# Kernel optimization log

Measured on AMD Instinct MI355X. Metric: run time of the kernel, lower is better.

Reference implementation:

```python
import jax, jax.numpy as jnp
import numpy as np

N_NODES = 50000
N_EDGES = 600000
D_IN = 44


def _glorot(key, shape):
    fan_in = shape[0]
    return jax.random.normal(key, shape, jnp.float32) * (1.0 / np.sqrt(fan_in))


def setup_inputs() -> dict:
    key = jax.random.key(0)
    ks = jax.random.split(key, 12)
    x = jax.random.normal(ks[0], (N_NODES, D_IN), jnp.float32)
    edge_index = jax.random.randint(ks[1], (2, N_EDGES), 0, N_NODES, dtype=jnp.int64)
    return {
        "x": x,
        "edge_index": edge_index,
        "W1": _glorot(ks[2], (D_IN, 128)),  "b1": jnp.zeros((128,), jnp.float32),
        "W2": _glorot(ks[3], (128, 64)),    "b2": jnp.zeros((64,), jnp.float32),
        "W3": _glorot(ks[4], (64, 32)),     "b3": jnp.zeros((32,), jnp.float32),
        "Wf1": _glorot(ks[5], (32, 16)),    "bf1": jnp.zeros((16,), jnp.float32),
        "Wf2": _glorot(ks[6], (16, 1)),     "bf2": jnp.zeros((1,), jnp.float32),
    }


def _gcn_conv(x, W, b, src, dst, norm, n):
    # GCNConv: h = x @ W; out_i = sum_{j->i} norm_ij * h_j  (self-loops included in src/dst)
    h = x @ W
    msg = h[src] * norm[:, None]              # [E+N, d_out] gather + scale
    out = jax.ops.segment_sum(msg, dst, num_segments=n)  # scatter-add
    return out + b


def reference(x, edge_index, W1, b1, W2, b2, W3, b3, Wf1, bf1, Wf2, bf2):
    n = x.shape[0]
    loop = jnp.arange(n, dtype=edge_index.dtype)
    src = jnp.concatenate([edge_index[0], loop])
    dst = jnp.concatenate([edge_index[1], loop])
    # symmetric normalization deg^-1/2 A_hat deg^-1/2 (deg includes self-loops)
    deg = jax.ops.segment_sum(jnp.ones_like(dst, dtype=x.dtype), dst, num_segments=n)
    dinv = jax.lax.rsqrt(jnp.maximum(deg, 1.0))
    norm = dinv[src] * dinv[dst]

    h = jax.nn.relu(_gcn_conv(x, W1, b1, src, dst, norm, n))
    h = jax.nn.relu(_gcn_conv(h, W2, b2, src, dst, norm, n))
    h = jax.nn.relu(_gcn_conv(h, W3, b3, src, dst, norm, n))
    h = jax.nn.relu(h @ Wf1 + bf1)
    return jax.nn.sigmoid(h @ Wf2 + bf2)
```

## Files before the change

### kernel.cpp

```cpp
#include <hip/hip_runtime.h>
#include <hip/hip_bf16.h>
#include <hip/hip_fp16.h>
#include <math.h>

#define N_NODES 50000
#define N_EDGES 600000
#define D_IN    44


__device__ __forceinline__ unsigned pack_bf2(float a, float b) {
    unsigned ua = __float_as_uint(a);
    ua = (ua + 0x7fffu + ((ua >> 16) & 1u)) >> 16;
    unsigned ub = __float_as_uint(b);
    ub = (ub + 0x7fffu + ((ub >> 16) & 1u)) & 0xffff0000u;
    return ua | ub;
}

#define BL(u) __uint_as_float((u) << 16)
#define BH(u) __uint_as_float((u) & 0xffff0000u)


__global__ void k_packx(const float* __restrict__ x, unsigned* __restrict__ xh,
                        int npairs, int* __restrict__ degc, int n) {
    int i = blockIdx.x * blockDim.x + threadIdx.x;
    if (i < npairs) {
        float2 v = ((const float2*)x)[i];
        xh[i] = pack_bf2(v.x, v.y);
    }
    if (i < n) degc[i] = 0;
}

__global__ void k_count(const int* __restrict__ dst, int* degc, int e) {
    int i = blockIdx.x * blockDim.x + threadIdx.x;
    if (i < e) atomicAdd(&degc[dst[i]], 1);
}

__global__ void k_blocksum(const int* __restrict__ degc, int* __restrict__ bsum, int n) {
    int i = blockIdx.x * 256 + threadIdx.x;
    int v = (i < n) ? degc[i] : 0;
    #pragma unroll
    for (int off = 32; off > 0; off >>= 1) v += __shfl_down(v, off, 64);
    __shared__ int ws[4];
    if ((threadIdx.x & 63) == 0) ws[threadIdx.x >> 6] = v;
    __syncthreads();
    if (threadIdx.x == 0) bsum[blockIdx.x] = ws[0] + ws[1] + ws[2] + ws[3];
}

__global__ void k_rowptr(const int* __restrict__ degc, const int* __restrict__ bsum,
                         int* __restrict__ row_ptr, int* __restrict__ cursor,
                         float* __restrict__ dinv, int n, int nb) {
    __shared__ int sb[256];
    __shared__ int s[256];
    int t = threadIdx.x;

    int bv = (t < nb) ? bsum[t] : 0;
    sb[t] = bv;
    __syncthreads();
    #pragma unroll
    for (int off = 1; off < 256; off <<= 1) {
        int u = (t >= off) ? sb[t - off] : 0;
        __syncthreads();
        sb[t] += u;
        __syncthreads();
    }
    int prefix = (blockIdx.x == 0) ? 0 : sb[blockIdx.x - 1];

    int i = blockIdx.x * 256 + t;
    int d = (i < n) ? degc[i] : 0;
    s[t] = d;
    __syncthreads();
    #pragma unroll
    for (int off = 1; off < 256; off <<= 1) {
        int u = (t >= off) ? s[t - off] : 0;
        __syncthreads();
        s[t] += u;
        __syncthreads();
    }
    int ex = s[t] - d + prefix;
    if (i < n) {
        row_ptr[i] = ex;
        cursor[i]  = ex;
        dinv[i]    = rsqrtf(1.0f + (float)d);
        if (i == n - 1) row_ptr[n] = ex + d;
    }
}

__global__ void k_fill(const int* __restrict__ src, const int* __restrict__ dst,
                       const float* __restrict__ dinv, int* cursor,
                       unsigned* __restrict__ csr_ew, int e) {
    int i = blockIdx.x * blockDim.x + threadIdx.x;
    if (i < e) {
        int s = src[i], d = dst[i];
        int p = atomicAdd(&cursor[d], 1);
        __half h = __float2half(dinv[s] * dinv[d]);
        csr_ew[p] = (unsigned)s | ((unsigned)__half_as_ushort(h) << 16);
    }
}


#define AGG_EDGE_HDR(EW, lo, hi)                                                \
            unsigned e0 = EW[min(k + 0, (hi) - 1)];                             \
            unsigned e1 = EW[min(k + 1, (hi) - 1)];                             \
            unsigned e2 = EW[min(k + 2, (hi) - 1)];                             \
            unsigned e3 = EW[min(k + 3, (hi) - 1)];                             \
            unsigned e4 = EW[min(k + 4, (hi) - 1)];                             \
            unsigned e5 = EW[min(k + 5, (hi) - 1)];                             \
            unsigned e6 = EW[min(k + 6, (hi) - 1)];                             \
            unsigned e7 = EW[min(k + 7, (hi) - 1)];                             \
            float w0 = __half2float(__ushort_as_half((unsigned short)(e0 >> 16)));                     \
            float w1 = (k + 1 < (hi)) ? __half2float(__ushort_as_half((unsigned short)(e1 >> 16))) : 0.0f;\
            float w2 = (k + 2 < (hi)) ? __half2float(__ushort_as_half((unsigned short)(e2 >> 16))) : 0.0f;\
            float w3 = (k + 3 < (hi)) ? __half2float(__ushort_as_half((unsigned short)(e3 >> 16))) : 0.0f;\
            float w4 = (k + 4 < (hi)) ? __half2float(__ushort_as_half((unsigned short)(e4 >> 16))) : 0.0f;\
            float w5 = (k + 5 < (hi)) ? __half2float(__ushort_as_half((unsigned short)(e5 >> 16))) : 0.0f;\
            float w6 = (k + 6 < (hi)) ? __half2float(__ushort_as_half((unsigned short)(e6 >> 16))) : 0.0f;\
            float w7 = (k + 7 < (hi)) ? __half2float(__ushort_as_half((unsigned short)(e7 >> 16))) : 0.0f;


#define AGG_ACC(tv, wv)                                   \
        acc.x += wv * BL(tv.x);                           \
        acc.y += wv * BH(tv.x);                           \
        acc.z += wv * BL(tv.y);                           \
        acc.w += wv * BH(tv.y);

#define AGG_BODY(T2, W4, lo, hi, j, acc, EW)                                    \
    {                                                                           \
        for (int k = (lo); k < (hi); k += 8) {                                  \
            AGG_EDGE_HDR(EW, lo, hi)                                            \
            uint2 t0 = T2[(size_t)(e0 & 0xffffu) * (W4) + (j)];                 \
            uint2 t1 = T2[(size_t)(e1 & 0xffffu) * (W4) + (j)];                 \
            uint2 t2 = T2[(size_t)(e2 & 0xffffu) * (W4) + (j)];                 \
            uint2 t3 = T2[(size_t)(e3 & 0xffffu) * (W4) + (j)];                 \
            uint2 t4 = T2[(size_t)(e4 & 0xffffu) * (W4) + (j)];                 \
            uint2 t5 = T2[(size_t)(e5 & 0xffffu) * (W4) + (j)];                 \
            uint2 t6 = T2[(size_t)(e6 & 0xffffu) * (W4) + (j)];                 \
            uint2 t7 = T2[(size_t)(e7 & 0xffffu) * (W4) + (j)];                 \
            AGG_ACC(t0, w0) AGG_ACC(t1, w1) AGG_ACC(t2, w2) AGG_ACC(t3, w3)     \
            AGG_ACC(t4, w4) AGG_ACC(t5, w5) AGG_ACC(t6, w6) AGG_ACC(t7, w7)     \
        }                                                                       \
    }


#define AGG_ACC4(tv, wv)                                  \
        a0.x += wv * BL(tv.x); a0.y += wv * BH(tv.x);     \
        a0.z += wv * BL(tv.y); a0.w += wv * BH(tv.y);     \
        a1.x += wv * BL(tv.z); a1.y += wv * BH(tv.z);     \
        a1.z += wv * BL(tv.w); a1.w += wv * BH(tv.w);

#define AGG_BODY4(T4, W4, lo, hi, j, EW)                                        \
    {                                                                           \
        for (int k = (lo); k < (hi); k += 8) {                                  \
            AGG_EDGE_HDR(EW, lo, hi)                                            \
            uint4 t0 = T4[(size_t)(e0 & 0xffffu) * (W4) + (j)];                 \
            uint4 t1 = T4[(size_t)(e1 & 0xffffu) * (W4) + (j)];                 \
            uint4 t2 = T4[(size_t)(e2 & 0xffffu) * (W4) + (j)];                 \
            uint4 t3 = T4[(size_t)(e3 & 0xffffu) * (W4) + (j)];                 \
            uint4 t4 = T4[(size_t)(e4 & 0xffffu) * (W4) + (j)];                 \
            uint4 t5 = T4[(size_t)(e5 & 0xffffu) * (W4) + (j)];                 \
            uint4 t6 = T4[(size_t)(e6 & 0xffffu) * (W4) + (j)];                 \
            uint4 t7 = T4[(size_t)(e7 & 0xffffu) * (W4) + (j)];                 \
            AGG_ACC4(t0, w0) AGG_ACC4(t1, w1) AGG_ACC4(t2, w2) AGG_ACC4(t3, w3) \
            AGG_ACC4(t4, w4) AGG_ACC4(t5, w5) AGG_ACC4(t6, w6) AGG_ACC4(t7, w7) \
        }                                                                       \
    }


#define AGG1_ECAP 1536

__global__ void k_agg1(const unsigned* __restrict__ T, const float* __restrict__ dinv,
                       const int* __restrict__ row_ptr, const unsigned* __restrict__ csr_ew,
                       unsigned short* __restrict__ O, int n) {
    __shared__ unsigned csr_s[AGG1_ECAP];
    const int t = threadIdx.x;
    const int base = blockIdx.x * 256;
    const int g0 = base / 11;
    const int glast = min((base + 255) / 11, n - 1);
    const int lo_blk = row_ptr[g0];
    const int nume = row_ptr[glast + 1] - lo_blk;
    const unsigned* ep;
    if (nume <= AGG1_ECAP) {
        for (int i = t; i < nume; i += 256) csr_s[i] = csr_ew[lo_blk + i];
        ep = csr_s;
    } else {
        ep = csr_ew + lo_blk;
    }
    __syncthreads();

    int idx = base + t;
    if (idx >= n * 11) return;
    int g = idx / 11;
    int j = idx - g * 11;

    const uint2* T2 = (const uint2*)T;
    float di = dinv[g];
    float sw = di * di;
    uint2 sv = T2[(size_t)g * 11 + j];
    float4 acc;
    acc.x = sw * BL(sv.x);
    acc.y = sw * BH(sv.x);
    acc.z = sw * BL(sv.y);
    acc.w = sw * BH(sv.y);
    int lo = row_ptr[g] - lo_blk;
    int hi = row_ptr[g + 1] - lo_blk;
    AGG_BODY(T2, 11, lo, hi, j, acc, ep)
    uint2 o;
    o.x = pack_bf2(acc.x, acc.y);
    o.y = pack_bf2(acc.z, acc.w);
    ((uint2*)O)[(size_t)g * 11 + j] = o;
}


template<int DI, int DO, int CT, bool BIAS_RELU, bool IN_BF16, bool OUT_BF16>
__global__ void k_gemm(const void* __restrict__ Xv, const float* __restrict__ W,
                       const float* __restrict__ b, void* __restrict__ H, int n) {
    const int ct0 = blockIdx.y * CT;
    int node = blockIdx.x * blockDim.x + threadIdx.x;
    if (node >= n) return;

    float acc[CT];
    #pragma unroll
    for (int c = 0; c < CT; ++c) acc[c] = BIAS_RELU ? b[ct0 + c] : 0.0f;

    const float* Wb = W + ct0;
    #pragma unroll
    for (int k0 = 0; k0 < DI / 4; ++k0) {
        float x0, x1, x2, x3;
        if (IN_BF16) {
            uint2 xv = ((const uint2*)((const unsigned short*)Xv + (size_t)node * DI))[k0];
            x0 = BL(xv.x); x1 = BH(xv.x); x2 = BL(xv.y); x3 = BH(xv.y);
        } else {
            float4 xv = ((const float4*)((const float*)Xv + (size_t)node * DI))[k0];
            x0 = xv.x; x1 = xv.y; x2 = xv.z; x3 = xv.w;
        }
        #pragma unroll
        for (int c = 0; c < CT; ++c) acc[c] += x0 * Wb[(k0 * 4 + 0) * DO + c];
        #pragma unroll
        for (int c = 0; c < CT; ++c) acc[c] += x1 * Wb[(k0 * 4 + 1) * DO + c];
        #pragma unroll
        for (int c = 0; c < CT; ++c) acc[c] += x2 * Wb[(k0 * 4 + 2) * DO + c];
        #pragma unroll
        for (int c = 0; c < CT; ++c) acc[c] += x3 * Wb[(k0 * 4 + 3) * DO + c];
    }

    #pragma unroll
    for (int c4 = 0; c4 < CT / 4; ++c4) {
        float4 v;
        v.x = acc[c4 * 4 + 0]; v.y = acc[c4 * 4 + 1];
        v.z = acc[c4 * 4 + 2]; v.w = acc[c4 * 4 + 3];
        if (BIAS_RELU) {
            v.x = fmaxf(v.x, 0.0f); v.y = fmaxf(v.y, 0.0f);
            v.z = fmaxf(v.z, 0.0f); v.w = fmaxf(v.w, 0.0f);
        }
        if (OUT_BF16) {
            uint2 p;
            p.x = pack_bf2(v.x, v.y);
            p.y = pack_bf2(v.z, v.w);
            ((uint2*)((unsigned short*)H + (size_t)node * DO + ct0))[c4] = p;
        } else {
            ((float4*)((float*)H + (size_t)node * DO + ct0))[c4] = v;
        }
    }
}


#define F23_ECAP 2048

__global__ void __launch_bounds__(256) k_fused23(
        const unsigned* __restrict__ T, const float* __restrict__ dinv,
        const int* __restrict__ row_ptr, const unsigned* __restrict__ csr_ew,
        const float* __restrict__ b2, const float* __restrict__ W3,
        unsigned short* __restrict__ outH, int n) {
    __shared__ unsigned csr_s[F23_ECAP];
    __shared__ float Xs[32 * 68];
    const int t = threadIdx.x;
    const int m = t >> 3;
    const int j = t & 7;
    const int g = blockIdx.x * 32 + m;
    const int gm = min(g, n - 1);

    const int g0 = blockIdx.x * 32;
    const int glast = min(g0 + 31, n - 1);
    const int lo_blk = row_ptr[g0];
    const int nume = row_ptr[glast + 1] - lo_blk;
    const unsigned* ep;
    if (nume <= F23_ECAP) {
        for (int i = t; i < nume; i += 256) csr_s[i] = csr_ew[lo_blk + i];
        ep = csr_s;
    } else {
        ep = csr_ew + lo_blk;
    }
    __syncthreads();

    const uint4* T4 = (const uint4*)T;
    {
        float di = dinv[gm];
        float sw = di * di;
        uint4 sv = T4[(size_t)gm * 8 + j];
        float4 a0, a1;
        a0.x = sw * BL(sv.x); a0.y = sw * BH(sv.x);
        a0.z = sw * BL(sv.y); a0.w = sw * BH(sv.y);
        a1.x = sw * BL(sv.z); a1.y = sw * BH(sv.z);
        a1.z = sw * BL(sv.w); a1.w = sw * BH(sv.w);
        int lo = row_ptr[gm] - lo_blk;
        int hi = row_ptr[gm + 1] - lo_blk;
        AGG_BODY4(T4, 8, lo, hi, j, ep)
        float4 bv0 = ((const float4*)b2)[2 * j];
        float4 bv1 = ((const float4*)b2)[2 * j + 1];
        a0.x = fmaxf(a0.x + bv0.x, 0.0f); a0.y = fmaxf(a0.y + bv0.y, 0.0f);
        a0.z = fmaxf(a0.z + bv0.z, 0.0f); a0.w = fmaxf(a0.w + bv0.w, 0.0f);
        a1.x = fmaxf(a1.x + bv1.x, 0.0f); a1.y = fmaxf(a1.y + bv1.y, 0.0f);
        a1.z = fmaxf(a1.z + bv1.z, 0.0f); a1.w = fmaxf(a1.w + bv1.w, 0.0f);
        *(float4*)&Xs[m * 68 + 8 * j]     = a0;
        *(float4*)&Xs[m * 68 + 8 * j + 4] = a1;
    }
    __syncthreads();

    {
        const int c = j * 4;
        float4 o = {0.0f, 0.0f, 0.0f, 0.0f};
        #pragma unroll 4
        for (int k4 = 0; k4 < 16; ++k4) {
            float4 xs = *(const float4*)&Xs[m * 68 + 4 * k4];
#define G3(hs, kk) { float4 wv = *(const float4*)&W3[(kk) * 32 + c];            \
            o.x += (hs) * wv.x; o.y += (hs) * wv.y;                             \
            o.z += (hs) * wv.z; o.w += (hs) * wv.w; }
            G3(xs.x, 4 * k4 + 0) G3(xs.y, 4 * k4 + 1)
            G3(xs.z, 4 * k4 + 2) G3(xs.w, 4 * k4 + 3)
#undef G3
        }
        if (g < n) {
            uint2 ov;
            ov.x = pack_bf2(o.x, o.y);
            ov.y = pack_bf2(o.z, o.w);
            *(uint2*)(outH + (size_t)g * 32 + c) = ov;
        }
    }
}


#define F3M_ECAP 2048

__global__ void __launch_bounds__(128) k_fused3m(
        const unsigned* __restrict__ T, const float* __restrict__ dinv,
        const int* __restrict__ row_ptr, const unsigned* __restrict__ csr_ew,
        const float* __restrict__ b3,
        const float* __restrict__ Wf1, const float* __restrict__ bf1,
        const float* __restrict__ Wf2, const float* __restrict__ bf2,
        float* __restrict__ out, int n) {
    __shared__ unsigned csr_s[F3M_ECAP];
    __shared__ float Xs[32 * 36];
    const int t = threadIdx.x;
    const int m = t >> 2;
    const int j = t & 3;
    const int g = blockIdx.x * 32 + m;
    const int gm = min(g, n - 1);

    const int g0 = blockIdx.x * 32;
    const int glast = min(g0 + 31, n - 1);
    const int lo_blk = row_ptr[g0];
    const int nume = row_ptr[glast + 1] - lo_blk;
    const unsigned* ep;
    if (nume <= F3M_ECAP) {
        for (int i = t; i < nume; i += 128) csr_s[i] = csr_ew[lo_blk + i];
        ep = csr_s;
    } else {
        ep = csr_ew + lo_blk;
    }
    __syncthreads();

    const uint4* T4 = (const uint4*)T;
    {
        float di = dinv[gm];
        float sw = di * di;
        uint4 sv = T4[(size_t)gm * 4 + j];
        float4 a0, a1;
        a0.x = sw * BL(sv.x); a0.y = sw * BH(sv.x);
        a0.z = sw * BL(sv.y); a0.w = sw * BH(sv.y);
        a1.x = sw * BL(sv.z); a1.y = sw * BH(sv.z);
        a1.z = sw * BL(sv.w); a1.w = sw * BH(sv.w);
        int lo = row_ptr[gm] - lo_blk;
        int hi = row_ptr[gm + 1] - lo_blk;
        AGG_BODY4(T4, 4, lo, hi, j, ep)
        float4 bv0 = ((const float4*)b3)[2 * j];
        float4 bv1 = ((const float4*)b3)[2 * j + 1];
        a0.x = fmaxf(a0.x + bv0.x, 0.0f); a0.y = fmaxf(a0.y + bv0.y, 0.0f);
        a0.z = fmaxf(a0.z + bv0.z, 0.0f); a0.w = fmaxf(a0.w + bv0.w, 0.0f);
        a1.x = fmaxf(a1.x + bv1.x, 0.0f); a1.y = fmaxf(a1.y + bv1.y, 0.0f);
        a1.z = fmaxf(a1.z + bv1.z, 0.0f); a1.w = fmaxf(a1.w + bv1.w, 0.0f);
        *(float4*)&Xs[m * 36 + 8 * j]     = a0;
        *(float4*)&Xs[m * 36 + 8 * j + 4] = a1;
    }
    __syncthreads();

    {
        const int c = j * 4;
        float4 h = *(const float4*)&bf1[c];
        #pragma unroll
        for (int k4 = 0; k4 < 8; ++k4) {
            float4 xs = *(const float4*)&Xs[m * 36 + 4 * k4];
#define FM(hs, kk) { float4 wv = *(const float4*)&Wf1[(kk) * 16 + c];           \
            h.x += (hs) * wv.x; h.y += (hs) * wv.y;                             \
            h.z += (hs) * wv.z; h.w += (hs) * wv.w; }
            FM(xs.x, 4 * k4 + 0) FM(xs.y, 4 * k4 + 1)
            FM(xs.z, 4 * k4 + 2) FM(xs.w, 4 * k4 + 3)
#undef FM
        }
        float4 w2 = *(const float4*)&Wf2[c];
        float p = fmaxf(h.x, 0.0f) * w2.x + fmaxf(h.y, 0.0f) * w2.y
                + fmaxf(h.z, 0.0f) * w2.z + fmaxf(h.w, 0.0f) * w2.w;
        p += __shfl_down(p, 2);
        p += __shfl_down(p, 1);
        if (j == 0 && g < n) out[g] = 1.0f / (1.0f + expf(-(p + bf2[0])));
    }
}


extern "C" void kernel_launch(void* const* d_in, const int* in_sizes, int n_in,
                              void* d_out, int out_size, void* d_ws, size_t ws_size,
                              hipStream_t stream) {
    const float* x   = (const float*)d_in[0];
    const int*   ei  = (const int*)d_in[1];
    const float* W1  = (const float*)d_in[2];
    const float* b1  = (const float*)d_in[3];
    const float* W2  = (const float*)d_in[4];
    const float* b2  = (const float*)d_in[5];
    const float* W3  = (const float*)d_in[6];
    const float* b3  = (const float*)d_in[7];
    const float* Wf1 = (const float*)d_in[8];
    const float* bf1 = (const float*)d_in[9];
    const float* Wf2 = (const float*)d_in[10];
    const float* bf2 = (const float*)d_in[11];
    float* out = (float*)d_out;

    const int N = N_NODES, E = N_EDGES;
    const int* src = ei;
    const int* dst = ei + E;

    const int B   = 256;
    const int NB  = (N + B - 1) / B;
    const int NBX = 200;

    char* w = (char*)d_ws;
    float*    dinv    = (float*)w;     w += (size_t)N * 4;
    int*      degc    = (int*)w;       w += (size_t)N * 4;
    int*      row_ptr = (int*)w;       w += (size_t)(N + 4) * 4;
    int*      cursor  = (int*)w;       w += (size_t)N * 4;
    int*      bsum    = (int*)w;       w += (size_t)256 * 4;
    unsigned* csr_ew  = (unsigned*)w;  w += (size_t)E * 4;
    unsigned* xh      = (unsigned*)w;  w += (size_t)N * 44 * 2;
    unsigned short* aggXh = (unsigned short*)w;  w += (size_t)N * 44 * 2;
    float*    buf1    = (float*)w;     w += (size_t)N * 128 * 4;
    unsigned short* bufAh = (unsigned short*)w;  w += (size_t)N * 64 * 2;
    unsigned short* bufBh = (unsigned short*)w;  w += (size_t)N * 32 * 2;

    k_packx    <<<(N * 22 + B - 1) / B, B, 0, stream>>>(x, xh, N * 22, degc, N);
    k_count    <<<(E + B - 1) / B, B, 0, stream>>>(dst, degc, E);
    k_blocksum <<<NB, B, 0, stream>>>(degc, bsum, N);
    k_rowptr   <<<NB, B, 0, stream>>>(degc, bsum, row_ptr, cursor, dinv, N, NB);
    k_fill     <<<(E + B - 1) / B, B, 0, stream>>>(src, dst, dinv, cursor, csr_ew, E);

    k_agg1<<<(N * 11 + B - 1) / B, B, 0, stream>>>(xh, dinv, row_ptr, csr_ew, aggXh, N);
    k_gemm<44, 128, 16, true, true, false><<<dim3(NBX, 8), B, 0, stream>>>(aggXh, W1, b1, buf1, N);
    k_gemm<128, 64, 16, false, false, true><<<dim3(NBX, 4), B, 0, stream>>>(buf1, W2, nullptr, bufAh, N);

    k_fused23<<<(N + 31) / 32, 256, 0, stream>>>((const unsigned*)bufAh, dinv, row_ptr,
                                                 csr_ew, b2, W3, bufBh, N);

    k_fused3m<<<(N + 31) / 32, 128, 0, stream>>>((const unsigned*)bufBh, dinv, row_ptr,
                                                 csr_ew, b3, Wf1, bf1, Wf2, bf2, out, N);
}
```

Measured before the change: 245.3 us.

## Fuse CSR build into cooperative kernel and fuse layer-1/2 GEMMs via LDS

Replaces five separate CSR-construction launches with one cooperative kernel that uses grid-wide syncs between packing, degree counting, the scan and the fill, and computes per-block sums with a second atomic. It also merges the two dense GEMMs into one kernel that keeps the 128-wide ReLU activations in shared memory instead of writing and rereading an fp32 buffer from global memory. This is meant to cut launch overhead and the global traffic of the intermediate. The cost is grid.sync latency, extra atomics on bsum, and shared-memory pressure that may lower occupancy in the fused GEMM.

Result: slower. 875.8 us (+257.0%).

```diff
diff --git a/kernel.cpp b/kernel.cpp
--- a/kernel.cpp
+++ b/kernel.cpp
@@ -1,11 +1,15 @@
 #include <hip/hip_runtime.h>
 #include <hip/hip_bf16.h>
 #include <hip/hip_fp16.h>
+#include <hip/hip_cooperative_groups.h>
 #include <math.h>
+
+namespace cg = cooperative_groups;
 
 #define N_NODES 50000
 #define N_EDGES 600000
 #define D_IN    44
+#define NB_CSR  196
 
 
 __device__ __forceinline__ unsigned pack_bf2(float a, float b) {
@@ -18,6 +22,78 @@
 
 #define BL(u) __uint_as_float((u) << 16)
 #define BH(u) __uint_as_float((u) & 0xffff0000u)
+
+
+__global__ void __launch_bounds__(256) k_csr(
+        const float* __restrict__ x, unsigned* __restrict__ xh,
+        const int* __restrict__ src, const int* __restrict__ dst,
+        int* __restrict__ degc, int* __restrict__ bsum,
+        int* __restrict__ row_ptr, int* __restrict__ cursor,
+        float* __restrict__ dinv, unsigned* __restrict__ csr_ew) {
+    cg::grid_group grid = cg::this_grid();
+    const int nth = gridDim.x * 256;
+    const int tid = blockIdx.x * 256 + threadIdx.x;
+
+    for (int i = tid; i < N_NODES; i += nth) degc[i] = 0;
+    if (tid < 256) bsum[tid] = 0;
+    for (int i = tid; i < N_NODES * 22; i += nth) {
+        float2 v = ((const float2*)x)[i];
+        xh[i] = pack_bf2(v.x, v.y);
+    }
+    grid.sync();
+
+    for (int i = tid; i < N_EDGES; i += nth) {
+        int d = dst[i];
+        atomicAdd(&degc[d], 1);
+        atomicAdd(&bsum[d >> 8], 1);
+    }
+    grid.sync();
+
+    if (blockIdx.x < NB_CSR) {
+        __shared__ int sb[256];
+        __shared__ int s[256];
+        int t = threadIdx.x;
+
+        int bv = (t < NB_CSR) ? bsum[t] : 0;
+        sb[t] = bv;
+        __syncthreads();
+        #pragma unroll
+        for (int off = 1; off < 256; off <<= 1) {
+            int u = (t >= off) ? sb[t - off] : 0;
+            __syncthreads();
+            sb[t] += u;
+            __syncthreads();
+        }
+        int prefix = (blockIdx.x == 0) ? 0 : sb[blockIdx.x - 1];
+
+        int i = blockIdx.x * 256 + t;
+        int d = (i < N_NODES) ? degc[i] : 0;
+        s[t] = d;
+        __syncthreads();
+        #pragma unroll
+        for (int off = 1; off < 256; off <<= 1) {
+            int u = (t >= off) ? s[t - off] : 0;
+            __syncthreads();
+            s[t] += u;
+            __syncthreads();
+        }
+        int ex = s[t] - d + prefix;
+        if (i < N_NODES) {
+            row_ptr[i] = ex;
+            cursor[i]  = ex;
+            dinv[i]    = rsqrtf(1.0f + (float)d);
+            if (i == N_NODES - 1) row_ptr[N_NODES] = ex + d;
+        }
+    }
+    grid.sync();
+
+    for (int i = tid; i < N_EDGES; i += nth) {
+        int sv = src[i], d = dst[i];
+        int p = atomicAdd(&cursor[d], 1);
+        __half h = __float2half(dinv[sv] * dinv[d]);
+        csr_ew[p] = (unsigned)sv | ((unsigned)__half_as_ushort(h) << 16);
+    }
+}
 
 
 __global__ void k_packx(const float* __restrict__ x, unsigned* __restrict__ xh,
@@ -116,7 +192,6 @@
             float w6 = (k + 6 < (hi)) ? __half2float(__ushort_as_half((unsigned short)(e6 >> 16))) : 0.0f;\
             float w7 = (k + 7 < (hi)) ? __half2float(__ushort_as_half((unsigned short)(e7 >> 16))) : 0.0f;
 
-
 #define AGG_ACC(tv, wv)                                   \
         acc.x += wv * BL(tv.x);                           \
         acc.y += wv * BH(tv.x);                           \
@@ -139,7 +214,6 @@
             AGG_ACC(t4, w4) AGG_ACC(t5, w5) AGG_ACC(t6, w6) AGG_ACC(t7, w7)     \
         }                                                                       \
     }
-
 
 #define AGG_ACC4(tv, wv)                                  \
         a0.x += wv * BL(tv.x); a0.y += wv * BH(tv.x);     \
@@ -210,54 +284,60 @@
 }
 
 
-template<int DI, int DO, int CT, bool BIAS_RELU, bool IN_BF16, bool OUT_BF16>
-__global__ void k_gemm(const void* __restrict__ Xv, const float* __restrict__ W,
-                       const float* __restrict__ b, void* __restrict__ H, int n) {
-    const int ct0 = blockIdx.y * CT;
-    int node = blockIdx.x * blockDim.x + threadIdx.x;
-    if (node >= n) return;
-
-    float acc[CT];
-    #pragma unroll
-    for (int c = 0; c < CT; ++c) acc[c] = BIAS_RELU ? b[ct0 + c] : 0.0f;
-
-    const float* Wb = W + ct0;
-    #pragma unroll
-    for (int k0 = 0; k0 < DI / 4; ++k0) {
-        float x0, x1, x2, x3;
-        if (IN_BF16) {
-            uint2 xv = ((const uint2*)((const unsigned short*)Xv + (size_t)node * DI))[k0];
-            x0 = BL(xv.x); x1 = BH(xv.x); x2 = BL(xv.y); x3 = BH(xv.y);
-        } else {
-            float4 xv = ((const float4*)((const float*)Xv + (size_t)node * DI))[k0];
-            x0 = xv.x; x1 = xv.y; x2 = xv.z; x3 = xv.w;
-        }
-        #pragma unroll
-        for (int c = 0; c < CT; ++c) acc[c] += x0 * Wb[(k0 * 4 + 0) * DO + c];
-        #pragma unroll
-        for (int c = 0; c < CT; ++c) acc[c] += x1 * Wb[(k0 * 4 + 1) * DO + c];
-        #pragma unroll
-        for (int c = 0; c < CT; ++c) acc[c] += x2 * Wb[(k0 * 4 + 2) * DO + c];
-        #pragma unroll
-        for (int c = 0; c < CT; ++c) acc[c] += x3 * Wb[(k0 * 4 + 3) * DO + c];
-    }
-
-    #pragma unroll
-    for (int c4 = 0; c4 < CT / 4; ++c4) {
-        float4 v;
-        v.x = acc[c4 * 4 + 0]; v.y = acc[c4 * 4 + 1];
-        v.z = acc[c4 * 4 + 2]; v.w = acc[c4 * 4 + 3];
-        if (BIAS_RELU) {
-            v.x = fmaxf(v.x, 0.0f); v.y = fmaxf(v.y, 0.0f);
-            v.z = fmaxf(v.z, 0.0f); v.w = fmaxf(v.w, 0.0f);
-        }
-        if (OUT_BF16) {
-            uint2 p;
-            p.x = pack_bf2(v.x, v.y);
-            p.y = pack_bf2(v.z, v.w);
-            ((uint2*)((unsigned short*)H + (size_t)node * DO + ct0))[c4] = p;
-        } else {
-            ((float4*)((float*)H + (size_t)node * DO + ct0))[c4] = v;
+__global__ void __launch_bounds__(256) k_gemm12(
+        const unsigned short* __restrict__ Xh, const float* __restrict__ W1,
+        const float* __restrict__ b1, const float* __restrict__ W2,
+        unsigned short* __restrict__ outH, int n) {
+    __shared__ float Xs[64 * 129];
+    const int t = threadIdx.x;
+    const int l = t & 63;
+    const int cgp = t >> 6;
+    const int g = blockIdx.x * 64 + l;
+    const int gm = min(g, n - 1);
+
+    {
+        const int c0 = cgp * 32;
+        float acc[32];
+        #pragma unroll
+        for (int i = 0; i < 32; ++i) acc[i] = b1[c0 + i];
+        const uint2* xr = (const uint2*)(Xh + (size_t)gm * 44);
+        #pragma unroll
+        for (int k0 = 0; k0 < 11; ++k0) {
+            uint2 xv = xr[k0];
+            float x0 = BL(xv.x), x1 = BH(xv.x), x2 = BL(xv.y), x3 = BH(xv.y);
+            #pragma unroll
+            for (int i = 0; i < 32; ++i) acc[i] += x0 * W1[(k0 * 4 + 0) * 128 + c0 + i];
+            #pragma unroll
+            for (int i = 0; i < 32; ++i) acc[i] += x1 * W1[(k0 * 4 + 1) * 128 + c0 + i];
+            #pragma unroll
+            for (int i = 0; i < 32; ++i) acc[i] += x2 * W1[(k0 * 4 + 2) * 128 + c0 + i];
+            #pragma unroll
+            for (int i = 0; i < 32; ++i) acc[i] += x3 * W1[(k0 * 4 + 3) * 128 + c0 + i];
+        }
+        #pragma unroll
+        for (int i = 0; i < 32; ++i) Xs[l * 129 + c0 + i] = fmaxf(acc[i], 0.0f);
+    }
+    __syncthreads();
+
+    {
+        const int c2 = cgp * 16;
+        float acc[16];
+        #pragma unroll
+        for (int i = 0; i < 16; ++i) acc[i] = 0.0f;
+        #pragma unroll 4
+        for (int k = 0; k < 128; ++k) {
+            float xs = Xs[l * 129 + k];
+            #pragma unroll
+            for (int i = 0; i < 16; ++i) acc[i] += xs * W2[k * 64 + c2 + i];
+        }
+        if (g < n) {
+            #pragma unroll
+            for (int q = 0; q < 4; ++q) {
+                uint2 p;
+                p.x = pack_bf2(acc[q * 4 + 0], acc[q * 4 + 1]);
+                p.y = pack_bf2(acc[q * 4 + 2], acc[q * 4 + 3]);
+                *(uint2*)(outH + (size_t)g * 64 + c2 + q * 4) = p;
+            }
         }
     }
 }
@@ -436,9 +516,8 @@
     const int* src = ei;
     const int* dst = ei + E;
 
-    const int B   = 256;
-    const int NB  = (N + B - 1) / B;
-    const int NBX = 200;
+    const int B  = 256;
+    const int NB = (N + B - 1) / B;
 
     char* w = (char*)d_ws;
     float*    dinv    = (float*)w;     w += (size_t)N * 4;
@@ -449,19 +528,26 @@
     unsigned* csr_ew  = (unsigned*)w;  w += (size_t)E * 4;
     unsigned* xh      = (unsigned*)w;  w += (size_t)N * 44 * 2;
     unsigned short* aggXh = (unsigned short*)w;  w += (size_t)N * 44 * 2;
-    float*    buf1    = (float*)w;     w += (size_t)N * 128 * 4;
     unsigned short* bufAh = (unsigned short*)w;  w += (size_t)N * 64 * 2;
     unsigned short* bufBh = (unsigned short*)w;  w += (size_t)N * 32 * 2;
 
-    k_packx    <<<(N * 22 + B - 1) / B, B, 0, stream>>>(x, xh, N * 22, degc, N);
-    k_count    <<<(E + B - 1) / B, B, 0, stream>>>(dst, degc, E);
-    k_blocksum <<<NB, B, 0, stream>>>(degc, bsum, N);
-    k_rowptr   <<<NB, B, 0, stream>>>(degc, bsum, row_ptr, cursor, dinv, N, NB);
-    k_fill     <<<(E + B - 1) / B, B, 0, stream>>>(src, dst, dinv, cursor, csr_ew, E);
+    {
+        void* cargs[] = { (void*)&x, (void*)&xh, (void*)&src, (void*)&dst,
+                          (void*)&degc, (void*)&bsum, (void*)&row_ptr,
+                          (void*)&cursor, (void*)&dinv, (void*)&csr_ew };
+        hipError_t cerr = hipLaunchCooperativeKernel((void*)k_csr, dim3(1024), dim3(256),
+                                                     cargs, 0, stream);
+        if (cerr != hipSuccess) {
+            k_packx    <<<(N * 22 + B - 1) / B, B, 0, stream>>>(x, xh, N * 22, degc, N);
+            k_count    <<<(E + B - 1) / B, B, 0, stream>>>(dst, degc, E);
+            k_blocksum <<<NB, B, 0, stream>>>(degc, bsum, N);
+            k_rowptr   <<<NB, B, 0, stream>>>(degc, bsum, row_ptr, cursor, dinv, N, NB);
+            k_fill     <<<(E + B - 1) / B, B, 0, stream>>>(src, dst, dinv, cursor, csr_ew, E);
+        }
+    }
 
     k_agg1<<<(N * 11 + B - 1) / B, B, 0, stream>>>(xh, dinv, row_ptr, csr_ew, aggXh, N);
-    k_gemm<44, 128, 16, true, true, false><<<dim3(NBX, 8), B, 0, stream>>>(aggXh, W1, b1, buf1, N);
-    k_gemm<128, 64, 16, false, false, true><<<dim3(NBX, 4), B, 0, stream>>>(buf1, W2, nullptr, bufAh, N);
+    k_gemm12<<<(N + 63) / 64, 256, 0, stream>>>(aggXh, W1, b1, W2, bufAh, N);
 
     k_fused23<<<(N + 31) / 32, 256, 0, stream>>>((const unsigned*)bufAh, dinv, row_ptr,
                                                  csr_ew, b2, W3, bufBh, N);
```
